# Kernel tuning notes

Measured on AMD Instinct MI355X. Metric: run time of the kernel, lower is better.

## Reference

```python
import jax, jax.numpy as jnp
import numpy as np

B, L, D = 2, 2048, 1024
H = 16
DH = D // H
FACTOR = 0.6
U = max(1, min(L, int(FACTOR * L)))  # 1228 selected queries


def setup_inputs() -> dict:
    key = jax.random.key(0)
    ks = jax.random.split(key, 9)
    s = 0.02
    return {
        "x": jax.random.normal(ks[0], (B, L, D), dtype=jnp.float32),
        "Wq": jax.random.normal(ks[1], (D, D), dtype=jnp.float32) * s,
        "bq": jnp.zeros((D,), dtype=jnp.float32),
        "Wk": jax.random.normal(ks[2], (D, D), dtype=jnp.float32) * s,
        "bk": jnp.zeros((D,), dtype=jnp.float32),
        "Wv": jax.random.normal(ks[3], (D, D), dtype=jnp.float32) * s,
        "bv": jnp.zeros((D,), dtype=jnp.float32),
        "Wo": jax.random.normal(ks[4], (D, D), dtype=jnp.float32) * s,
        "bo": jnp.zeros((D,), dtype=jnp.float32),
    }


def _split_heads(x):
    b, l, d = x.shape
    return x.reshape(b, l, H, DH).transpose(0, 2, 1, 3)  # [b,h,l,dh]


def reference(x, Wq, bq, Wk, bk, Wv, bv, Wo, bo):
    b, l, _ = x.shape
    scale = 1.0 / jnp.sqrt(jnp.asarray(DH, dtype=x.dtype))

    q = _split_heads(x @ Wq + bq)  # [b,h,l,dh]
    k = _split_heads(x @ Wk + bk)
    v = _split_heads(x @ Wv + bv)

    # full scores for sparsity heuristic
    scores = jnp.einsum("bhqd,bhkd->bhqk", q, k) * scale  # [b,h,l,l]
    sparsity = scores.max(axis=-1) - scores.mean(axis=-1)  # [b,h,l]

    _, top_idx = jax.lax.top_k(sparsity, U)  # [b,h,U]

    # gather selected queries, attend only on those rows
    q_sel = jnp.take_along_axis(q, top_idx[..., None], axis=2)  # [b,h,U,dh]
    scores_sel = jnp.einsum("bhud,bhkd->bhuk", q_sel, k) * scale  # [b,h,U,l]
    attn = jax.nn.softmax(scores_sel, axis=-1)
    out_sel = jnp.einsum("bhuk,bhkd->bhud", attn, v)  # [b,h,U,dh]

    # scatter back into zero-initialized output
    bi = jnp.arange(b)[:, None, None]
    hi = jnp.arange(H)[None, :, None]
    out = jnp.zeros_like(q).at[bi, hi, top_idx].set(out_sel)  # [b,h,l,dh]

    out = out.transpose(0, 2, 1, 3).reshape(b, l, D)
    return out @ Wo + bo
```

## Files before the change

kernel.cpp:

```cpp
#include <hip/hip_runtime.h>
#include <math.h>
#include <stdint.h>

#define Bn 2
#define Ln 2048
#define Dn 1024
#define Hn 16
#define DHn 64
#define Un 1228
#define BHn (Bn*Hn)
#define WIN 32
#define SCALE 0.125f
#define SXf 16.0f
#define SWf 256.0f
#define SQf 16.0f
#define SVf 16.0f
#define SPf 16.0f
#define ESC_PROJ (1.0f / 4096.0f)
#define ESC_OUT  (1.0f / 65536.0f)
#define PSC (SCALE / 256.0f)

typedef _Float16 f16;
typedef __attribute__((ext_vector_type(8))) _Float16 f16x8;
typedef __attribute__((ext_vector_type(4))) float f32x4;
struct h4s { f16 x, y, z, w; };

__device__ __forceinline__ void splitf16(float f, f16& hi, f16& lo) {
  hi = (f16)f;
  lo = (f16)(f - (float)hi);
}

__device__ __forceinline__ void gl_lds16(const void* g, void* l) {
  __builtin_amdgcn_global_load_lds(
      (const __attribute__((address_space(1))) void*)g,
      (__attribute__((address_space(3))) void*)l, 16, 0, 0);
}

#define MFMA(a, b, c) __builtin_amdgcn_mfma_f32_16x16x32_f16((a), (b), (c), 0, 0, 0)

__global__ __launch_bounds__(256) void split_kernel(
    const float* __restrict__ in, f16* __restrict__ oh, f16* __restrict__ ol, int n4) {
  int i = blockIdx.x * 256 + threadIdx.x;
  if (i >= n4) return;
  float4 v = ((const float4*)in)[i];
  h4s h, l;
  splitf16(v.x * SXf, h.x, l.x); splitf16(v.y * SXf, h.y, l.y);
  splitf16(v.z * SXf, h.z, l.z); splitf16(v.w * SXf, h.w, l.w);
  ((h4s*)oh)[i] = h; ((h4s*)ol)[i] = l;
}

__global__ __launch_bounds__(256) void tsplit_w4(
    const float* __restrict__ W0, const float* __restrict__ W1,
    const float* __restrict__ W2, const float* __restrict__ W3,
    f16* __restrict__ oh, f16* __restrict__ ol) {
  __shared__ float ts[64][65];
  const int t = threadIdx.x;
  const int r0 = blockIdx.x * 64, c0 = blockIdx.y * 64;
  const int z = blockIdx.z;
  const float* in = (z == 0) ? W0 : (z == 1) ? W1 : (z == 2) ? W2 : W3;
#pragma unroll
  for (int c = 0; c < 4; ++c) {
    int f = (c * 256 + t) * 4; int row = f >> 6, col = f & 63;
    float4 v = *(const float4*)&in[(size_t)(r0 + row) * Dn + c0 + col];
    ts[row][col] = v.x; ts[row][col + 1] = v.y; ts[row][col + 2] = v.z; ts[row][col + 3] = v.w;
  }
  __syncthreads();
#pragma unroll
  for (int c = 0; c < 4; ++c) {
    int f = (c * 256 + t) * 4; int crow = f >> 6, rcol = f & 63;
    h4s h, l;
    splitf16(ts[rcol + 0][crow] * SWf, h.x, l.x);
    splitf16(ts[rcol + 1][crow] * SWf, h.y, l.y);
    splitf16(ts[rcol + 2][crow] * SWf, h.z, l.z);
    splitf16(ts[rcol + 3][crow] * SWf, h.w, l.w);
    size_t o = (size_t)(z * 1024 + c0 + crow) * Dn + r0 + rcol;
    *(h4s*)&oh[o] = h; *(h4s*)&ol[o] = l;
  }
}

__global__ void gemm_qkv(
    const f16* __restrict__ Ah, const f16* __restrict__ Al,
    const f16* __restrict__ Bth, const f16* __restrict__ Btl,
    const float* __restrict__ bq, const float* __restrict__ bk, const float* __restrict__ bv,
    float* __restrict__ Qf, f16* __restrict__ Qbh,
    float* __restrict__ Kf, f16* __restrict__ Kbh,
    f16* __restrict__ Vh16, int K) {
  __shared__ f16 sAh[128 * 32], sAl[128 * 32], sBh[128 * 32], sBl[128 * 32];
  const int t = threadIdx.x;
  const int w = t >> 6, lane = t & 63, lm = lane & 15, q = lane >> 4;
  const int wr = w >> 1, wc = w & 1;
  const int n0 = blockIdx.x * 128, m0 = blockIdx.y * 128;
  f32x4 acc[4][4] = {};
  for (int k0 = 0; k0 < K; k0 += 32) {
    const f16* s0 = Ah + (size_t)m0 * K + k0;
    const f16* s1 = Al + (size_t)m0 * K + k0;
    const f16* s2 = Bth + (size_t)n0 * K + k0;
    const f16* s3 = Btl + (size_t)n0 * K + k0;
#pragma unroll
    for (int c = 0; c < 2; ++c) {
      int f = (c * 256 + t) * 8; int row = f >> 5, col = f & 31;
      size_t go = (size_t)row * K + col;
      gl_lds16(s0 + go, &sAh[f]);
      gl_lds16(s1 + go, &sAl[f]);
      gl_lds16(s2 + go, &sBh[f]);
      gl_lds16(s3 + go, &sBl[f]);
    }
    __syncthreads();
    f16x8 a_h[4], a_l[4], b_h[4], b_l[4];
#pragma unroll
    for (int mi = 0; mi < 4; ++mi) {
      int r = (wr * 64 + mi * 16 + lm) * 32 + q * 8;
      a_h[mi] = *(const f16x8*)&sAh[r];
      a_l[mi] = *(const f16x8*)&sAl[r];
    }
#pragma unroll
    for (int ni = 0; ni < 4; ++ni) {
      int r = (wc * 64 + ni * 16 + lm) * 32 + q * 8;
      b_h[ni] = *(const f16x8*)&sBh[r];
      b_l[ni] = *(const f16x8*)&sBl[r];
    }
#pragma unroll
    for (int mi = 0; mi < 4; ++mi)
#pragma unroll
      for (int ni = 0; ni < 4; ++ni) {
        acc[mi][ni] = MFMA(a_h[mi], b_h[ni], acc[mi][ni]);
        acc[mi][ni] = MFMA(a_h[mi], b_l[ni], acc[mi][ni]);
        acc[mi][ni] = MFMA(a_l[mi], b_h[ni], acc[mi][ni]);
      }
    __syncthreads();
  }
#pragma unroll
  for (int mi = 0; mi < 4; ++mi)
#pragma unroll
    for (int ni = 0; ni < 4; ++ni) {
      int nglob = n0 + wc * 64 + ni * 16;
      int seg = nglob >> 10;
      int c = (nglob & 1023) + lm;
      const float* bp = (seg == 0) ? bq : (seg == 1) ? bk : bv;
      float bvv = bp[c];
#pragma unroll
      for (int r = 0; r < 4; ++r) {
        int grow = m0 + wr * 64 + mi * 16 + q * 4 + r;
        float v = acc[mi][ni][r] * ESC_PROJ + bvv;
        size_t o = (size_t)grow * 1024 + c;
        if (seg == 0) {
          Qf[o] = v;
          Qbh[o] = (f16)(v * SQf);
        } else if (seg == 1) {
          Kf[o] = v;
          Kbh[o] = (f16)(v * SQf);
        } else {
          Vh16[o] = (f16)(v * SVf);
        }
      }
    }
}

__global__ __launch_bounds__(256) void tsplit_v(
    const f16* __restrict__ Vh16, f16* __restrict__ out) {
  __shared__ f16 ts[64][72];
  const int t = threadIdx.x;
  const int l0 = blockIdx.x * 64;
  const int bh = blockIdx.y, b = bh >> 4, h = bh & 15;
#pragma unroll
  for (int c = 0; c < 2; ++c) {
    int e = c * 256 + t; int row = e >> 3, cg = e & 7;
    *(uint4*)&ts[row][cg * 8] =
        *(const uint4*)&Vh16[((size_t)b * Ln + l0 + row) * Dn + h * DHn + cg * 8];
  }
  __syncthreads();
#pragma unroll
  for (int c = 0; c < 2; ++c) {
    int e = c * 256 + t; int drow = e >> 3, lg = e & 7;
    f16 tmp[8];
#pragma unroll
    for (int j = 0; j < 8; ++j) tmp[j] = ts[lg * 8 + j][drow];
    *(uint4*)&out[((size_t)bh * DHn + drow) * Ln + l0 + lg * 8] = *(uint4*)tmp;
  }
}

__global__ __launch_bounds__(256, 4) void gemm_a1(
    const f16* __restrict__ A,
    const f16* __restrict__ Bth, const f16* __restrict__ Btl,
    const float* __restrict__ bias, float escale,
    float* __restrict__ Cf, int M, int N, int K) {
  __shared__ f16 sA[128 * 32], sBh[64 * 32], sBl[64 * 32];
  const int t = threadIdx.x;
  const int w = t >> 6, lane = t & 63, lm = lane & 15, q = lane >> 4;
  const int wr = w >> 1, wc = w & 1;
  const int n0 = blockIdx.x * 64, m0 = blockIdx.y * 128;
  f32x4 acc[4][2] = {};
  for (int k0 = 0; k0 < K; k0 += 32) {
    const f16* s0 = A + (size_t)m0 * K + k0;
    const f16* s2 = Bth + (size_t)n0 * K + k0;
    const f16* s3 = Btl + (size_t)n0 * K + k0;
#pragma unroll
    for (int c = 0; c < 2; ++c) {
      int f = (c * 256 + t) * 8; int row = f >> 5, col = f & 31;
      gl_lds16(s0 + (size_t)row * K + col, &sA[f]);
    }
    {
      int f = t * 8; int row = f >> 5, col = f & 31;
      gl_lds16(s2 + (size_t)row * K + col, &sBh[f]);
      gl_lds16(s3 + (size_t)row * K + col, &sBl[f]);
    }
    __syncthreads();
    f16x8 a_[4], b_h[2], b_l[2];
#pragma unroll
    for (int mi = 0; mi < 4; ++mi)
      a_[mi] = *(const f16x8*)&sA[(wr * 64 + mi * 16 + lm) * 32 + q * 8];
#pragma unroll
    for (int ni = 0; ni < 2; ++ni) {
      int r = (wc * 32 + ni * 16 + lm) * 32 + q * 8;
      b_h[ni] = *(const f16x8*)&sBh[r];
      b_l[ni] = *(const f16x8*)&sBl[r];
    }
#pragma unroll
    for (int mi = 0; mi < 4; ++mi)
#pragma unroll
      for (int ni = 0; ni < 2; ++ni) {
        acc[mi][ni] = MFMA(a_[mi], b_h[ni], acc[mi][ni]);
        acc[mi][ni] = MFMA(a_[mi], b_l[ni], acc[mi][ni]);
      }
    __syncthreads();
  }
#pragma unroll
  for (int mi = 0; mi < 4; ++mi)
#pragma unroll
    for (int ni = 0; ni < 2; ++ni) {
      int gcol = n0 + wc * 32 + ni * 16 + lm;
      float bvv = bias[gcol];
#pragma unroll
      for (int r = 0; r < 4; ++r) {
        int grow = m0 + wr * 64 + mi * 16 + q * 4 + r;
        Cf[(size_t)grow * N + gcol] = acc[mi][ni][r] * escale + bvv;
      }
    }
}

__global__ __launch_bounds__(256) void ksum_part(
    const float* __restrict__ Kf, float* __restrict__ ksum) {
  __shared__ float red[4][64];
  const int t = threadIdx.x, d = t & 63, seg = t >> 6;
  const int bx = blockIdx.x, bh = blockIdx.y, b = bh >> 4, h = bh & 15;
  float s = 0.f;
  const int lbase = bx * 256 + seg * 64;
  for (int r = 0; r < 64; ++r)
    s += Kf[((size_t)b * Ln + lbase + r) * Dn + h * DHn + d];
  red[seg][d] = s;
  __syncthreads();
  if (t < 64) atomicAdd(&ksum[bh * DHn + t], red[0][t] + red[1][t] + red[2][t] + red[3][t]);
}

__global__ __launch_bounds__(256, 2) void attn_stats_mfma(
    const f16* __restrict__ Qh, const f16* __restrict__ Kh,
    const float* __restrict__ ksum,
    float* __restrict__ row_max, float* __restrict__ spars) {
  __shared__ f16 sQ[128 * 64], sK[128 * 64];
  __shared__ float redm[128][5];
  const int t = threadIdx.x;
  const int w = t >> 6, lane = t & 63, lm = lane & 15, q = lane >> 4;
  const int bh = blockIdx.y, b = bh >> 4, h = bh & 15;
  const int q0 = blockIdx.x * 128;
  const f16* qs = Qh + ((size_t)b * Ln + q0) * Dn + h * DHn;
#pragma unroll
  for (int c = 0; c < 4; ++c) {
    int f = (c * 256 + t) * 8; int row = f >> 6, col = f & 63;
    gl_lds16(qs + (size_t)row * Dn + col, &sQ[f]);
  }
  __syncthreads();
  f16x8 a_[8][2];
#pragma unroll
  for (int mi = 0; mi < 8; ++mi)
#pragma unroll
    for (int ks = 0; ks < 2; ++ks)
      a_[mi][ks] = *(const f16x8*)&sQ[(mi * 16 + lm) * 64 + ks * 32 + q * 8];
  float rmax[8][4];
#pragma unroll
  for (int mi = 0; mi < 8; ++mi)
#pragma unroll
    for (int r = 0; r < 4; ++r) rmax[mi][r] = -1e30f;

  for (int kt = 0; kt < Ln / 128; ++kt) {
    __syncthreads();
    const f16* ks_ = Kh + ((size_t)b * Ln + kt * 128) * Dn + h * DHn;
#pragma unroll
    for (int c = 0; c < 4; ++c) {
      int f = (c * 256 + t) * 8; int row = f >> 6, col = f & 63;
      gl_lds16(ks_ + (size_t)row * Dn + col, &sK[f]);
    }
    __syncthreads();
#pragma unroll
    for (int ni = 0; ni < 2; ++ni) {
      int bcol = (w * 2 + ni) * 16;
      f16x8 b_[2];
#pragma unroll
      for (int ks = 0; ks < 2; ++ks)
        b_[ks] = *(const f16x8*)&sK[(bcol + lm) * 64 + ks * 32 + q * 8];
#pragma unroll
      for (int mi = 0; mi < 8; ++mi) {
        f32x4 acc = {0.f, 0.f, 0.f, 0.f};
        acc = MFMA(a_[mi][0], b_[0], acc);
        acc = MFMA(a_[mi][1], b_[1], acc);
#pragma unroll
        for (int r = 0; r < 4; ++r) rmax[mi][r] = fmaxf(rmax[mi][r], acc[r]);
      }
    }
  }
#pragma unroll
  for (int mi = 0; mi < 8; ++mi)
#pragma unroll
    for (int r = 0; r < 4; ++r) {
      float v = rmax[mi][r];
      v = fmaxf(v, __shfl_xor(v, 1)); v = fmaxf(v, __shfl_xor(v, 2));
      v = fmaxf(v, __shfl_xor(v, 4)); v = fmaxf(v, __shfl_xor(v, 8));
      if (lm == 0) redm[mi * 16 + q * 4 + r][w] = v;
    }
  __syncthreads();
  if (t < 128) {
    float m = fmaxf(fmaxf(redm[t][0], redm[t][1]), fmaxf(redm[t][2], redm[t][3]));
    float dot = 0.f;
    const float* kp = ksum + bh * DHn;
#pragma unroll
    for (int d = 0; d < 64; ++d)
      dot += (float)sQ[t * 64 + d] * kp[d];
    row_max[(size_t)bh * Ln + q0 + t] = m * PSC;
    spars[(size_t)bh * Ln + q0 + t] = m * PSC - dot * (SCALE / (16.0f * (float)Ln));
  }
}

__global__ __launch_bounds__(1024) void topk_sort(
    const float* __restrict__ spars, int* __restrict__ top_idx, int* __restrict__ wrow) {
  __shared__ unsigned long long keys[Ln];
  const int t = threadIdx.x;
  const int bh = blockIdx.x;
  for (int i = t; i < Ln; i += 1024) {
    unsigned u = __float_as_uint(spars[(size_t)bh * Ln + i]);
    u = (u & 0x80000000u) ? ~u : (u | 0x80000000u);
    u = ~u;
    keys[i] = ((unsigned long long)u << 32) | (unsigned)i;
  }
  __syncthreads();
  for (int k = 2; k <= Ln; k <<= 1) {
    for (int j = k >> 1; j > 0; j >>= 1) {
      int i = ((t & ~(j - 1)) << 1) | (t & (j - 1));
      int ixj = i | j;
      unsigned long long a = keys[i], bb = keys[ixj];
      bool up = ((i & k) == 0);
      if ((a > bb) == up) { keys[i] = bb; keys[ixj] = a; }
      __syncthreads();
    }
  }
  for (int u = t; u < Un - WIN / 2; u += 1024)
    top_idx[(size_t)bh * Un + u] = (int)(keys[u] & 0xFFFFFFFFu);
  if (t < WIN) wrow[bh * WIN + t] = (int)(keys[Un - WIN / 2 + t] & 0xFFFFFFFFu);
}

__global__ __launch_bounds__(256) void refine_rows(
    const float* __restrict__ Qf, const float* __restrict__ Kf,
    const int* __restrict__ wrow, float* __restrict__ spx) {
  __shared__ float qs[4][68];
  __shared__ float Ks[64][68];
  __shared__ float redm[4][64], reds[4][64];
  const int t = threadIdx.x;
  const int g = blockIdx.x, bh = blockIdx.y, b = bh >> 4, h = bh & 15;
  const int j = t & 3, s = t >> 2;
  if (t < 256) {
    int jj = t >> 6, d = t & 63;
    int qi = wrow[bh * WIN + g * 4 + jj];
    qs[jj][d] = Qf[((size_t)b * Ln + qi) * Dn + h * DHn + d];
  }
  float mx = -1e30f, sm = 0.f;
  for (int kt = 0; kt < Ln / 64; ++kt) {
    __syncthreads();
#pragma unroll
    for (int c = 0; c < 4; ++c) {
      int idx = c * 256 + t;
      int krow = idx >> 4, kc4 = idx & 15;
      *(float4*)&Ks[krow][kc4 * 4] =
          *(const float4*)&Kf[((size_t)b * Ln + kt * 64 + krow) * Dn + h * DHn + kc4 * 4];
    }
    __syncthreads();
    float acc = 0.f;
#pragma unroll
    for (int c = 0; c < 16; ++c) {
      float4 k4 = *(const float4*)&Ks[s][c * 4];
      float4 q4 = *(const float4*)&qs[j][c * 4];
      acc = fmaf(k4.x, q4.x, acc);
      acc = fmaf(k4.y, q4.y, acc);
      acc = fmaf(k4.z, q4.z, acc);
      acc = fmaf(k4.w, q4.w, acc);
    }
    mx = fmaxf(mx, acc); sm += acc;
  }
  redm[j][s] = mx; reds[j][s] = sm;
  __syncthreads();
  if (t < 4) {
    float m = -1e30f, ssum = 0.f;
    for (int k = 0; k < 64; ++k) { m = fmaxf(m, redm[t][k]); ssum += reds[t][k]; }
    spx[bh * WIN + g * 4 + t] = SCALE * (m - ssum * (1.0f / (float)Ln));
  }
}

__global__ __launch_bounds__(64) void topk_final(
    const float* __restrict__ spx, const int* __restrict__ wrow,
    int* __restrict__ top_idx) {
  const int bh = blockIdx.x;
  if (threadIdx.x != 0) return;
  float v[WIN]; int r[WIN];
#pragma unroll
  for (int j = 0; j < WIN; ++j) { v[j] = spx[bh * WIN + j]; r[j] = wrow[bh * WIN + j]; }
  unsigned taken = 0;
  for (int s = 0; s < WIN / 2; ++s) {
    int best = -1;
    for (int j = 0; j < WIN; ++j) {
      if (taken & (1u << j)) continue;
      if (best < 0 || v[j] > v[best] || (v[j] == v[best] && r[j] < r[best])) best = j;
    }
    taken |= 1u << best;
    top_idx[(size_t)bh * Un + (Un - WIN / 2) + s] = r[best];
  }
}

__global__ __launch_bounds__(256, 4) void attn_sel_part(
    const f16* __restrict__ Qh, const f16* __restrict__ Kh,
    const f16* __restrict__ Vth,
    const int* __restrict__ topi, const float* __restrict__ row_max,
    float* __restrict__ pO, float* __restrict__ pD) {
  __shared__ f16 sK[64 * 64], sV[64 * 64];
  __shared__ f16 sQP[64 * 80];
  __shared__ float rmL[64];
  __shared__ int qxL[64];
  __shared__ float dred[64][5];
  const int t = threadIdx.x;
  const int w = t >> 6, lane = t & 63, lm = lane & 15, q = lane >> 4;
  const int half = blockIdx.y & 1, bh = blockIdx.y >> 1, b = bh >> 4, h = bh & 15;
  const int u0 = blockIdx.x * 64;
  const int nrows = (Un - u0 < 64) ? (Un - u0) : 64;
  if (t < 64) {
    int qi = topi[(size_t)bh * Un + ((t < nrows) ? (u0 + t) : 0)];
    qxL[t] = qi;
    rmL[t] = row_max[(size_t)bh * Ln + qi];
  }
  __syncthreads();
#pragma unroll
  for (int c = 0; c < 2; ++c) {
    int f = (c * 256 + t) * 8; int row = f >> 6, col = f & 63;
    size_t go = ((size_t)b * Ln + qxL[row]) * Dn + h * DHn + col;
    *(uint4*)&sQP[row * 80 + col] = *(const uint4*)&Qh[go];
  }
  __syncthreads();
  f16x8 aq[4][2];
#pragma unroll
  for (int mi = 0; mi < 4; ++mi)
#pragma unroll
    for (int ks = 0; ks < 2; ++ks)
      aq[mi][ks] = *(const f16x8*)&sQP[(mi * 16 + lm) * 80 + ks * 32 + q * 8];
  f32x4 oacc[4] = {};
  float dacc[4][4] = {};

  const f16* kbase = Kh + (size_t)b * Ln * Dn + h * DHn;
  const f16* vbase = Vth + (size_t)bh * DHn * Ln;
  for (int kt = 0; kt < 16; ++kt) {
    const int l0 = half * 1024 + kt * 64;
    __syncthreads();
#pragma unroll
    for (int c = 0; c < 2; ++c) {
      int f = (c * 256 + t) * 8; int row = f >> 6, col = f & 63;
      gl_lds16(kbase + (size_t)(l0 + row) * Dn + col, &sK[f]);
      gl_lds16(vbase + (size_t)row * Ln + l0 + col, &sV[f]);
    }
    __syncthreads();
    f16x8 kb[2];
#pragma unroll
    for (int ks = 0; ks < 2; ++ks)
      kb[ks] = *(const f16x8*)&sK[(w * 16 + lm) * 64 + ks * 32 + q * 8];
#pragma unroll
    for (int mi = 0; mi < 4; ++mi) {
      f32x4 acc = {0.f, 0.f, 0.f, 0.f};
      acc = MFMA(aq[mi][0], kb[0], acc);
      acc = MFMA(aq[mi][1], kb[1], acc);
#pragma unroll
      for (int r = 0; r < 4; ++r) {
        int row = mi * 16 + q * 4 + r;
        float p = __expf(acc[r] * PSC - rmL[row]);
        dacc[mi][r] += p;
        sQP[row * 80 + w * 16 + lm] = (f16)(p * SPf);
      }
    }
    __syncthreads();
    f16x8 vb[2];
#pragma unroll
    for (int ks = 0; ks < 2; ++ks)
      vb[ks] = *(const f16x8*)&sV[(w * 16 + lm) * 64 + ks * 32 + q * 8];
#pragma unroll
    for (int mi = 0; mi < 4; ++mi) {
#pragma unroll
      for (int ks = 0; ks < 2; ++ks) {
        f16x8 pf = *(const f16x8*)&sQP[(mi * 16 + lm) * 80 + ks * 32 + q * 8];
        oacc[mi] = MFMA(pf, vb[ks], oacc[mi]);
      }
    }
  }
#pragma unroll
  for (int mi = 0; mi < 4; ++mi)
#pragma unroll
    for (int r = 0; r < 4; ++r) {
      float v = dacc[mi][r];
      v += __shfl_xor(v, 1); v += __shfl_xor(v, 2);
      v += __shfl_xor(v, 4); v += __shfl_xor(v, 8);
      if (lm == 0) dred[mi * 16 + q * 4 + r][w] = v;
    }
  __syncthreads();
  const size_t pbase = ((size_t)half * BHn + bh) * 1280 + u0;
  if (t < 64)
    pD[pbase + t] = dred[t][0] + dred[t][1] + dred[t][2] + dred[t][3];
#pragma unroll
  for (int mi = 0; mi < 4; ++mi)
#pragma unroll
    for (int r = 0; r < 4; ++r) {
      int row = mi * 16 + q * 4 + r;
      pO[(pbase + row) * 64 + w * 16 + lm] = oacc[mi][r];
    }
}

__global__ __launch_bounds__(256) void attn_combine(
    const float* __restrict__ pO, const float* __restrict__ pD,
    const int* __restrict__ topi, f16* __restrict__ AOh) {
  const int t = threadIdx.x;
  const int u0 = blockIdx.x * 64, bh = blockIdx.y, b = bh >> 4, h = bh & 15;
  const int nrows = (Un - u0 < 64) ? (Un - u0) : 64;
  const int row = t >> 2, pg = t & 3;
  if (row >= nrows) return;
  int qi = topi[(size_t)bh * Un + u0 + row];
  size_t i0 = (size_t)bh * 1280 + u0 + row;
  size_t i1 = (size_t)BHn * 1280 + i0;
  float dinv = 1.0f / (pD[i0] + pD[i1]);
  const float* p0 = &pO[i0 * 64 + pg * 16];
  const float* p1 = &pO[i1 * 64 + pg * 16];
  f16 buf[16];
#pragma unroll
  for (int c = 0; c < 4; ++c) {
    float4 a = *(const float4*)&p0[c * 4];
    float4 bb = *(const float4*)&p1[c * 4];
    buf[c * 4 + 0] = (f16)((a.x + bb.x) * dinv);
    buf[c * 4 + 1] = (f16)((a.y + bb.y) * dinv);
    buf[c * 4 + 2] = (f16)((a.z + bb.z) * dinv);
    buf[c * 4 + 3] = (f16)((a.w + bb.w) * dinv);
  }
  f16* dst = &AOh[((size_t)b * Ln + qi) * Dn + h * DHn + pg * 16];
  *(uint4*)&dst[0] = *(uint4*)&buf[0];
  *(uint4*)&dst[8] = *(uint4*)&buf[8];
}

extern "C" void kernel_launch(void* const* d_in, const int* in_sizes, int n_in,
                              void* d_out, int out_size, void* d_ws, size_t ws_size,
                              hipStream_t stream) {
  (void)in_sizes; (void)n_in; (void)out_size; (void)ws_size;
  const float* x  = (const float*)d_in[0];
  const float* Wq = (const float*)d_in[1];
  const float* bq = (const float*)d_in[2];
  const float* Wk = (const float*)d_in[3];
  const float* bk = (const float*)d_in[4];
  const float* Wv = (const float*)d_in[5];
  const float* bv = (const float*)d_in[6];
  const float* Wo = (const float*)d_in[7];
  const float* bo = (const float*)d_in[8];
  float* out = (float*)d_out;

  uint8_t* p = (uint8_t*)d_ws;
  const size_t NE = (size_t)Bn * Ln * Dn;
  f16* xh = (f16*)p;  p += NE * 2;
  f16* xl = (f16*)p;  p += NE * 2;
  f16* Wt_h = (f16*)p; p += (size_t)4096 * Dn * 2;
  f16* Wt_l = (f16*)p; p += (size_t)4096 * Dn * 2;
  f16* Qbh = (f16*)p; p += NE * 2;
  f16* Kbh = (f16*)p; p += NE * 2;
  float* Qf = (float*)p;  p += NE * 4;
  float* Kf = (float*)p;  p += NE * 4;
  f16* Vh16 = (f16*)p; p += NE * 2;
  f16* Vth  = (f16*)p; p += NE * 2;
  float* rowmax = (float*)p; p += (size_t)BHn * Ln * 4;
  float* spars  = (float*)p; p += (size_t)BHn * Ln * 4;
  float* ksum   = (float*)p; p += (size_t)BHn * DHn * 4;
  int* topi     = (int*)p;   p += (size_t)BHn * Un * 4;
  int* wrow     = (int*)p;   p += (size_t)BHn * WIN * 4;
  float* spx    = (float*)p; p += (size_t)BHn * WIN * 4;
  float* pD     = (float*)p; p += (size_t)2 * BHn * 1280 * 4;
  float* pO = Qf;
  f16* AOh = xh;

  dim3 blk(256);
  hipLaunchKernelGGL(split_kernel, dim3((int)(NE / 4 / 256)), blk, 0, stream, x, xh, xl, (int)(NE / 4));
  hipLaunchKernelGGL(tsplit_w4, dim3(16, 16, 4), blk, 0, stream, Wq, Wk, Wv, Wo, Wt_h, Wt_l);
  hipLaunchKernelGGL(gemm_qkv, dim3(24, 32), blk, 0, stream, xh, xl, Wt_h, Wt_l,
                     bq, bk, bv, Qf, Qbh, Kf, Kbh, Vh16, Dn);
  hipLaunchKernelGGL(tsplit_v, dim3(Ln / 64, BHn), blk, 0, stream, Vh16, Vth);
  hipMemsetAsync(ksum, 0, (size_t)BHn * DHn * 4, stream);
  hipLaunchKernelGGL(ksum_part, dim3(8, BHn), blk, 0, stream, Kf, ksum);
  hipLaunchKernelGGL(attn_stats_mfma, dim3(Ln / 128, BHn), blk, 0, stream,
                     Qbh, Kbh, ksum, rowmax, spars);
  hipLaunchKernelGGL(topk_sort, dim3(BHn), dim3(1024), 0, stream, spars, topi, wrow);
  hipLaunchKernelGGL(refine_rows, dim3(WIN / 4, BHn), blk, 0, stream, Qf, Kf, wrow, spx);
  hipLaunchKernelGGL(topk_final, dim3(BHn), dim3(64), 0, stream, spx, wrow, topi);
  hipMemsetAsync(AOh, 0, NE * 2, stream);
  hipLaunchKernelGGL(attn_sel_part, dim3((Un + 63) / 64, 2 * BHn), blk, 0, stream,
                     Qbh, Kbh, Vth, topi, rowmax, pO, pD);
  hipLaunchKernelGGL(attn_combine, dim3((Un + 63) / 64, BHn), blk, 0, stream,
                     pO, pD, topi, AOh);
  hipLaunchKernelGGL(gemm_a1, dim3(16, 32), blk, 0, stream, AOh,
                     Wt_h + (size_t)3072 * Dn, Wt_l + (size_t)3072 * Dn, bo,
                     ESC_OUT, out, Bn * Ln, Dn, Dn);
}
```

Measured before the change: 421.4 us.

## Drop split-precision for Q, V and output GEMMs; recompute boundary-window queries in fp32

The QKV GEMM now runs the three-MFMA hi/lo split only for the K segment. Q and V use a single fp16 MFMA, and the output projection drops the low weight half. The full fp32 Q buffer is gone; instead a new kernel recomputes fp32 Q rows only for the top-k boundary window, which is widened from 32 to 64 candidates. The final boundary selection is rewritten as a parallel rank count. This cuts MFMA work and memory traffic, at the cost of lower precision in Q, V and the output, which the wider refinement window is meant to offset.

```diff
diff --git a/kernel.cpp b/kernel.cpp
--- a/kernel.cpp
+++ b/kernel.cpp
@@ -9,7 +9,7 @@
 #define DHn 64
 #define Un 1228
 #define BHn (Bn*Hn)
-#define WIN 32
+#define WIN 64
 #define SCALE 0.125f
 #define SXf 16.0f
 #define SWf 256.0f
@@ -74,7 +74,8 @@
     splitf16(ts[rcol + 2][crow] * SWf, h.z, l.z);
     splitf16(ts[rcol + 3][crow] * SWf, h.w, l.w);
     size_t o = (size_t)(z * 1024 + c0 + crow) * Dn + r0 + rcol;
-    *(h4s*)&oh[o] = h; *(h4s*)&ol[o] = l;
+    *(h4s*)&oh[o] = h;
+    if (z == 1) *(h4s*)&ol[o] = l;
   }
 }
 
@@ -82,7 +83,7 @@
     const f16* __restrict__ Ah, const f16* __restrict__ Al,
     const f16* __restrict__ Bth, const f16* __restrict__ Btl,
     const float* __restrict__ bq, const float* __restrict__ bk, const float* __restrict__ bv,
-    float* __restrict__ Qf, f16* __restrict__ Qbh,
+    f16* __restrict__ Qbh,
     float* __restrict__ Kf, f16* __restrict__ Kbh,
     f16* __restrict__ Vh16, int K) {
   __shared__ f16 sAh[128 * 32], sAl[128 * 32], sBh[128 * 32], sBl[128 * 32];
@@ -90,6 +91,7 @@
   const int w = t >> 6, lane = t & 63, lm = lane & 15, q = lane >> 4;
   const int wr = w >> 1, wc = w & 1;
   const int n0 = blockIdx.x * 128, m0 = blockIdx.y * 128;
+  const int seg = blockIdx.x >> 3;
   f32x4 acc[4][4] = {};
   for (int k0 = 0; k0 < K; k0 += 32) {
     const f16* s0 = Ah + (size_t)m0 * K + k0;
@@ -101,9 +103,11 @@
       int f = (c * 256 + t) * 8; int row = f >> 5, col = f & 31;
       size_t go = (size_t)row * K + col;
       gl_lds16(s0 + go, &sAh[f]);
-      gl_lds16(s1 + go, &sAl[f]);
       gl_lds16(s2 + go, &sBh[f]);
-      gl_lds16(s3 + go, &sBl[f]);
+      if (seg == 1) {
+        gl_lds16(s1 + go, &sAl[f]);
+        gl_lds16(s3 + go, &sBl[f]);
+      }
     }
     __syncthreads();
     f16x8 a_h[4], a_l[4], b_h[4], b_l[4];
@@ -111,22 +115,30 @@
     for (int mi = 0; mi < 4; ++mi) {
       int r = (wr * 64 + mi * 16 + lm) * 32 + q * 8;
       a_h[mi] = *(const f16x8*)&sAh[r];
-      a_l[mi] = *(const f16x8*)&sAl[r];
+      if (seg == 1) a_l[mi] = *(const f16x8*)&sAl[r];
     }
 #pragma unroll
     for (int ni = 0; ni < 4; ++ni) {
       int r = (wc * 64 + ni * 16 + lm) * 32 + q * 8;
       b_h[ni] = *(const f16x8*)&sBh[r];
-      b_l[ni] = *(const f16x8*)&sBl[r];
-    }
-#pragma unroll
-    for (int mi = 0; mi < 4; ++mi)
-#pragma unroll
-      for (int ni = 0; ni < 4; ++ni) {
-        acc[mi][ni] = MFMA(a_h[mi], b_h[ni], acc[mi][ni]);
-        acc[mi][ni] = MFMA(a_h[mi], b_l[ni], acc[mi][ni]);
-        acc[mi][ni] = MFMA(a_l[mi], b_h[ni], acc[mi][ni]);
-      }
+      if (seg == 1) b_l[ni] = *(const f16x8*)&sBl[r];
+    }
+    if (seg == 1) {
+#pragma unroll
+      for (int mi = 0; mi < 4; ++mi)
+#pragma unroll
+        for (int ni = 0; ni < 4; ++ni) {
+          acc[mi][ni] = MFMA(a_h[mi], b_h[ni], acc[mi][ni]);
+          acc[mi][ni] = MFMA(a_h[mi], b_l[ni], acc[mi][ni]);
+          acc[mi][ni] = MFMA(a_l[mi], b_h[ni], acc[mi][ni]);
+        }
+    } else {
+#pragma unroll
+      for (int mi = 0; mi < 4; ++mi)
+#pragma unroll
+        for (int ni = 0; ni < 4; ++ni)
+          acc[mi][ni] = MFMA(a_h[mi], b_h[ni], acc[mi][ni]);
+    }
     __syncthreads();
   }
 #pragma unroll
@@ -134,7 +146,6 @@
 #pragma unroll
     for (int ni = 0; ni < 4; ++ni) {
       int nglob = n0 + wc * 64 + ni * 16;
-      int seg = nglob >> 10;
       int c = (nglob & 1023) + lm;
       const float* bp = (seg == 0) ? bq : (seg == 1) ? bk : bv;
       float bvv = bp[c];
@@ -144,7 +155,6 @@
         float v = acc[mi][ni][r] * ESC_PROJ + bvv;
         size_t o = (size_t)grow * 1024 + c;
         if (seg == 0) {
-          Qf[o] = v;
           Qbh[o] = (f16)(v * SQf);
         } else if (seg == 1) {
           Kf[o] = v;
@@ -180,11 +190,10 @@
 }
 
 __global__ __launch_bounds__(256, 4) void gemm_a1(
-    const f16* __restrict__ A,
-    const f16* __restrict__ Bth, const f16* __restrict__ Btl,
+    const f16* __restrict__ A, const f16* __restrict__ Bth,
     const float* __restrict__ bias, float escale,
     float* __restrict__ Cf, int M, int N, int K) {
-  __shared__ f16 sA[128 * 32], sBh[64 * 32], sBl[64 * 32];
+  __shared__ f16 sA[128 * 32], sB[64 * 32];
   const int t = threadIdx.x;
   const int w = t >> 6, lane = t & 63, lm = lane & 15, q = lane >> 4;
   const int wr = w >> 1, wc = w & 1;
@@ -193,7 +202,6 @@
   for (int k0 = 0; k0 < K; k0 += 32) {
     const f16* s0 = A + (size_t)m0 * K + k0;
     const f16* s2 = Bth + (size_t)n0 * K + k0;
-    const f16* s3 = Btl + (size_t)n0 * K + k0;
 #pragma unroll
     for (int c = 0; c < 2; ++c) {
       int f = (c * 256 + t) * 8; int row = f >> 5, col = f & 31;
@@ -201,27 +209,21 @@
     }
     {
       int f = t * 8; int row = f >> 5, col = f & 31;
-      gl_lds16(s2 + (size_t)row * K + col, &sBh[f]);
-      gl_lds16(s3 + (size_t)row * K + col, &sBl[f]);
-    }
-    __syncthreads();
-    f16x8 a_[4], b_h[2], b_l[2];
+      gl_lds16(s2 + (size_t)row * K + col, &sB[f]);
+    }
+    __syncthreads();
+    f16x8 a_[4], b_[2];
 #pragma unroll
     for (int mi = 0; mi < 4; ++mi)
       a_[mi] = *(const f16x8*)&sA[(wr * 64 + mi * 16 + lm) * 32 + q * 8];
 #pragma unroll
-    for (int ni = 0; ni < 2; ++ni) {
-      int r = (wc * 32 + ni * 16 + lm) * 32 + q * 8;
-      b_h[ni] = *(const f16x8*)&sBh[r];
-      b_l[ni] = *(const f16x8*)&sBl[r];
-    }
+    for (int ni = 0; ni < 2; ++ni)
+      b_[ni] = *(const f16x8*)&sB[(wc * 32 + ni * 16 + lm) * 32 + q * 8];
 #pragma unroll
     for (int mi = 0; mi < 4; ++mi)
 #pragma unroll
-      for (int ni = 0; ni < 2; ++ni) {
-        acc[mi][ni] = MFMA(a_[mi], b_h[ni], acc[mi][ni]);
-        acc[mi][ni] = MFMA(a_[mi], b_l[ni], acc[mi][ni]);
-      }
+      for (int ni = 0; ni < 2; ++ni)
+        acc[mi][ni] = MFMA(a_[mi], b_[ni], acc[mi][ni]);
     __syncthreads();
   }
 #pragma unroll
@@ -356,19 +358,52 @@
   if (t < WIN) wrow[bh * WIN + t] = (int)(keys[Un - WIN / 2 + t] & 0xFFFFFFFFu);
 }
 
+__global__ __launch_bounds__(256) void window_q(
+    const float* __restrict__ x, const float* __restrict__ Wq, const float* __restrict__ bq,
+    const int* __restrict__ wrow, float* __restrict__ qx) {
+  __shared__ float xs[16][68];
+  __shared__ int wr_[16];
+  const int t = threadIdx.x;
+  const int jg = blockIdx.x * 16;
+  const int bh = blockIdx.y, b = bh >> 4, h = bh & 15;
+  const int d = t & 63, rg = t >> 6;
+  if (t < 16) wr_[t] = wrow[bh * WIN + jg + t];
+  __syncthreads();
+  float acc[4] = {};
+  for (int kc = 0; kc < Dn; kc += 64) {
+    {
+      int row = t >> 4, col = (t & 15) * 4;
+      *(float4*)&xs[row][col] = *(const float4*)&x[((size_t)b * Ln + wr_[row]) * Dn + kc + col];
+    }
+    __syncthreads();
+#pragma unroll 8
+    for (int kk = 0; kk < 64; ++kk) {
+      float wv = Wq[(size_t)(kc + kk) * Dn + h * DHn + d];
+      acc[0] = fmaf(xs[rg * 4 + 0][kk], wv, acc[0]);
+      acc[1] = fmaf(xs[rg * 4 + 1][kk], wv, acc[1]);
+      acc[2] = fmaf(xs[rg * 4 + 2][kk], wv, acc[2]);
+      acc[3] = fmaf(xs[rg * 4 + 3][kk], wv, acc[3]);
+    }
+    __syncthreads();
+  }
+  float bqs = bq[h * DHn + d];
+#pragma unroll
+  for (int rr = 0; rr < 4; ++rr)
+    qx[((size_t)bh * WIN + jg + rg * 4 + rr) * 64 + d] = acc[rr] + bqs;
+}
+
 __global__ __launch_bounds__(256) void refine_rows(
-    const float* __restrict__ Qf, const float* __restrict__ Kf,
-    const int* __restrict__ wrow, float* __restrict__ spx) {
+    const float* __restrict__ qx, const float* __restrict__ Kf,
+    float* __restrict__ spx) {
   __shared__ float qs[4][68];
   __shared__ float Ks[64][68];
   __shared__ float redm[4][64], reds[4][64];
   const int t = threadIdx.x;
   const int g = blockIdx.x, bh = blockIdx.y, b = bh >> 4, h = bh & 15;
   const int j = t & 3, s = t >> 2;
-  if (t < 256) {
+  {
     int jj = t >> 6, d = t & 63;
-    int qi = wrow[bh * WIN + g * 4 + jj];
-    qs[jj][d] = Qf[((size_t)b * Ln + qi) * Dn + h * DHn + d];
+    qs[jj][d] = qx[((size_t)bh * WIN + g * 4 + jj) * 64 + d];
   }
   float mx = -1e30f, sm = 0.f;
   for (int kt = 0; kt < Ln / 64; ++kt) {
@@ -405,21 +440,16 @@
 __global__ __launch_bounds__(64) void topk_final(
     const float* __restrict__ spx, const int* __restrict__ wrow,
     int* __restrict__ top_idx) {
-  const int bh = blockIdx.x;
-  if (threadIdx.x != 0) return;
-  float v[WIN]; int r[WIN];
-#pragma unroll
-  for (int j = 0; j < WIN; ++j) { v[j] = spx[bh * WIN + j]; r[j] = wrow[bh * WIN + j]; }
-  unsigned taken = 0;
-  for (int s = 0; s < WIN / 2; ++s) {
-    int best = -1;
-    for (int j = 0; j < WIN; ++j) {
-      if (taken & (1u << j)) continue;
-      if (best < 0 || v[j] > v[best] || (v[j] == v[best] && r[j] < r[best])) best = j;
-    }
-    taken |= 1u << best;
-    top_idx[(size_t)bh * Un + (Un - WIN / 2) + s] = r[best];
-  }
+  __shared__ float v[WIN];
+  __shared__ int r[WIN];
+  const int bh = blockIdx.x, j = threadIdx.x;
+  v[j] = spx[bh * WIN + j];
+  r[j] = wrow[bh * WIN + j];
+  __syncthreads();
+  int rank = 0;
+  for (int i = 0; i < WIN; ++i)
+    rank += (v[i] > v[j]) || (v[i] == v[j] && r[i] < r[j]);
+  if (rank < WIN / 2) top_idx[(size_t)bh * Un + (Un - WIN / 2) + rank] = r[j];
 }
 
 __global__ __launch_bounds__(256, 4) void attn_sel_part(
@@ -576,7 +606,6 @@
   f16* Wt_l = (f16*)p; p += (size_t)4096 * Dn * 2;
   f16* Qbh = (f16*)p; p += NE * 2;
   f16* Kbh = (f16*)p; p += NE * 2;
-  float* Qf = (float*)p;  p += NE * 4;
   float* Kf = (float*)p;  p += NE * 4;
   f16* Vh16 = (f16*)p; p += NE * 2;
   f16* Vth  = (f16*)p; p += NE * 2;
@@ -586,29 +615,30 @@
   int* topi     = (int*)p;   p += (size_t)BHn * Un * 4;
   int* wrow     = (int*)p;   p += (size_t)BHn * WIN * 4;
   float* spx    = (float*)p; p += (size_t)BHn * WIN * 4;
+  float* qx     = (float*)p; p += (size_t)BHn * WIN * 64 * 4;
   float* pD     = (float*)p; p += (size_t)2 * BHn * 1280 * 4;
-  float* pO = Qf;
+  float* pO     = (float*)p; p += (size_t)2 * BHn * 1280 * 64 * 4;
   f16* AOh = xh;
 
   dim3 blk(256);
   hipLaunchKernelGGL(split_kernel, dim3((int)(NE / 4 / 256)), blk, 0, stream, x, xh, xl, (int)(NE / 4));
   hipLaunchKernelGGL(tsplit_w4, dim3(16, 16, 4), blk, 0, stream, Wq, Wk, Wv, Wo, Wt_h, Wt_l);
   hipLaunchKernelGGL(gemm_qkv, dim3(24, 32), blk, 0, stream, xh, xl, Wt_h, Wt_l,
-                     bq, bk, bv, Qf, Qbh, Kf, Kbh, Vh16, Dn);
+                     bq, bk, bv, Qbh, Kf, Kbh, Vh16, Dn);
   hipLaunchKernelGGL(tsplit_v, dim3(Ln / 64, BHn), blk, 0, stream, Vh16, Vth);
   hipMemsetAsync(ksum, 0, (size_t)BHn * DHn * 4, stream);
   hipLaunchKernelGGL(ksum_part, dim3(8, BHn), blk, 0, stream, Kf, ksum);
   hipLaunchKernelGGL(attn_stats_mfma, dim3(Ln / 128, BHn), blk, 0, stream,
                      Qbh, Kbh, ksum, rowmax, spars);
   hipLaunchKernelGGL(topk_sort, dim3(BHn), dim3(1024), 0, stream, spars, topi, wrow);
-  hipLaunchKernelGGL(refine_rows, dim3(WIN / 4, BHn), blk, 0, stream, Qf, Kf, wrow, spx);
-  hipLaunchKernelGGL(topk_final, dim3(BHn), dim3(64), 0, stream, spx, wrow, topi);
+  hipLaunchKernelGGL(window_q, dim3(WIN / 16, BHn), blk, 0, stream, x, Wq, bq, wrow, qx);
+  hipLaunchKernelGGL(refine_rows, dim3(WIN / 4, BHn), blk, 0, stream, qx, Kf, spx);
+  hipLaunchKernelGGL(topk_final, dim3(BHn), dim3(WIN), 0, stream, spx, wrow, topi);
   hipMemsetAsync(AOh, 0, NE * 2, stream);
   hipLaunchKernelGGL(attn_sel_part, dim3((Un + 63) / 64, 2 * BHn), blk, 0, stream,
                      Qbh, Kbh, Vth, topi, rowmax, pO, pD);
   hipLaunchKernelGGL(attn_combine, dim3((Un + 63) / 64, BHn), blk, 0, stream,
                      pO, pD, topi, AOh);
   hipLaunchKernelGGL(gemm_a1, dim3(16, 32), blk, 0, stream, AOh,
-                     Wt_h + (size_t)3072 * Dn, Wt_l + (size_t)3072 * Dn, bo,
-                     ESC_OUT, out, Bn * Ln, Dn, Dn);
-}
+                     Wt_h + (size_t)3072 * Dn, bo, ESC_OUT, out, Bn * Ln, Dn, Dn);
+}
```

New measurement: 923.5 us. 119% more time.
